# Kernel tuning notes

Hardware: AMD Instinct MI355X
Metric: run time of the kernel (lower is better)

The kernel has to match this reference:

```python
import jax, jax.numpy as jnp
import numpy as np

B, T, H, WD = 512, 168, 512, 4  # batch, seq_len, hidden_dim, WEATHER_DIM


def setup_inputs() -> dict:
    key = jax.random.key(0)
    ks = jax.random.split(key, 11)
    sc = 1.0 / np.sqrt(H)

    def u(k, shape):
        return jax.random.uniform(k, shape, jnp.float32, -sc, sc)

    return {
        "inputs": jax.random.normal(ks[0], (B, T, WD + 1), dtype=jnp.float32),
        # layer 1: input_sz=1 (counts)
        "W1": u(ks[1], (1, 4 * H)),
        "U1": u(ks[2], (H, 4 * H)),
        "V1": u(ks[3], (WD, 4 * H)),
        "b1": u(ks[4], (4 * H,)),
        # layer 2: input_sz=H
        "W2": u(ks[5], (H, 4 * H)),
        "U2": u(ks[6], (H, 4 * H)),
        "V2": u(ks[7], (WD, 4 * H)),
        "b2": u(ks[8], (4 * H,)),
        # final linear head (xavier-ish init)
        "fc_w": u(ks[9], (1, H)),
        "fc_b": jnp.zeros((1,), jnp.float32),
    }


def pew_lstm(x, w, W, U, V, b):
    """Weather-conditioned LSTM layer.
    x: [B,T,I] main input, w: [B,T,WD] weather.
    Gates = x@W + h@U + weather@V + b (weather injected each step).
    Returns hidden sequence [B,T,H]."""
    bs = x.shape[0]
    hdim = U.shape[0]
    # precompute all non-recurrent contributions once: [B,T,4H]
    pre = jnp.einsum('bti,ig->btg', x, W) + jnp.einsum('btw,wg->btg', w, V) + b

    def step(carry, pre_t):
        h, c = carry
        gates = pre_t + h @ U              # [B,4H]
        i, f, g, o = jnp.split(gates, 4, axis=-1)
        c = jax.nn.sigmoid(f) * c + jax.nn.sigmoid(i) * jnp.tanh(g)
        h = jax.nn.sigmoid(o) * jnp.tanh(c)
        return (h, c), h

    h0 = jnp.zeros((bs, hdim), x.dtype)
    (_, _), hs = jax.lax.scan(step, (h0, h0), pre.transpose(1, 0, 2))
    return hs.transpose(1, 0, 2)  # [B,T,H]


def reference(inputs, W1, U1, V1, b1, W2, U2, V2, b2, fc_w, fc_b):
    weather = inputs[:, :, :-1]   # [B,T,WD]
    counts = inputs[:, :, -1:]    # [B,T,1]
    h1 = pew_lstm(counts, weather, W1, U1, V1, b1)
    h2 = pew_lstm(h1, weather, W2, U2, V2, b2)
    out = h2.reshape(-1, h2.shape[-1]) @ fc_w.T + fc_b  # [B*T,1]
    return out.reshape(-1)
```

## Files before the change

kernel.cpp:

```cpp
#include <hip/hip_runtime.h>
#include <cstdint>
#include <cstddef>

typedef unsigned int   u32;
typedef unsigned short u16;
typedef unsigned long long u64;
typedef __attribute__((ext_vector_type(8))) short bf16x8;
typedef __attribute__((ext_vector_type(4))) float f32x4;

#define B_  512
#define T_  168
#define H_  512

#define OFF_U1P   (0u)
#define OFF_UW2P  (2u*1024*1024)
#define OFF_FLAGS (6u*1024*1024)
#define OFF_H2R   (6u*1024*1024 + 512u*1024)
#define OFF_H1_R9 (8u*1024*1024)
#define OFF_H2_R9 (12u*1024*1024)
#define OFF_H1F   (8u*1024*1024)
#define SLOT_B    (524288u)
#define OFF_H2F   (OFF_H1F + 168u*SLOT_B)
#define H_SLOT    262144u
#define NRING     8
#define FS        32
#define SMEM_SZ   (131072 + 6144 + 3072)

__device__ __forceinline__ u16 f2bf(float v){
  u32 u = __float_as_uint(v);
  return (u16)((u + 0x7fffu + ((u >> 16) & 1u)) >> 16);
}
__device__ __forceinline__ float sigm_f(float x){ return __fdividef(1.f, 1.f + __expf(-x)); }
__device__ __forceinline__ float tanh_ff(float x){
  float e = __expf(-2.f*fabsf(x));
  float t = __fdividef(1.f - e, 1.f + e);
  return (x < 0.f) ? -t : t;
}
__device__ __forceinline__ void async_cp16(const void* g, void* l){
  __builtin_amdgcn_global_load_lds((const __attribute__((address_space(1))) u32*)g,
                                   (__attribute__((address_space(3))) u32*)l, 16, 0, 0);
}
__device__ __forceinline__ void drain_vm(){
  asm volatile("s_waitcnt vmcnt(0)" ::: "memory");
}
__device__ __forceinline__ void wpoll(const int* p, bool act, int target, int& vlast){
  if (__all((!act) || (vlast >= target))) return;
  while (true){
    int v = 0x7fffffff;
    if (act) v = __hip_atomic_load(p, __ATOMIC_RELAXED, __HIP_MEMORY_SCOPE_AGENT);
    if (__all(v >= target)){ vlast = v; break; }
    __builtin_amdgcn_s_sleep(1);
  }
}
template<bool PLAIN>
__device__ __forceinline__ bf16x8 ldh(const u16* p){
  if (PLAIN) return *(const bf16x8*)p;
  union { u64 q[2]; bf16x8 v; } u;
  u.q[0] = __hip_atomic_load((const u64*)p,     __ATOMIC_RELAXED, __HIP_MEMORY_SCOPE_AGENT);
  u.q[1] = __hip_atomic_load(((const u64*)p)+1, __ATOMIC_RELAXED, __HIP_MEMORY_SCOPE_AGENT);
  return u.v;
}
__device__ __forceinline__ void ring_st16(u16* p, uint4 v){
  u64 lo = ((u64)v.y << 32) | v.x;
  u64 hi = ((u64)v.w << 32) | v.z;
  __hip_atomic_store((u64*)p,     lo, __ATOMIC_RELAXED, __HIP_MEMORY_SCOPE_AGENT);
  __hip_atomic_store(((u64*)p)+1, hi, __ATOMIC_RELAXED, __HIP_MEMORY_SCOPE_AGENT);
}

__global__ void pack_w_kernel(const float* __restrict__ U1, const float* __restrict__ W2,
                              const float* __restrict__ U2, u16* __restrict__ U1p,
                              u16* __restrict__ UW2p)
{
  int idx = blockIdx.x*256 + threadIdx.x;
  int ln = idx & 63;
  int q8 = ((ln >> 4) << 3);
  int cl = ln & 15;
  if (idx < 16*128*64) {
    int kc = idx >> 13, ng = (idx >> 6) & 127;
    int row0 = kc*32 + q8, col = ng*16 + cl;
    u16* d = U1p + (size_t)idx*8;
    #pragma unroll
    for (int j=0;j<8;j++) d[j] = f2bf(U1[(size_t)(row0+j)*2048 + col]);
  } else {
    int i2 = idx - 16*128*64;
    if (i2 >= 32*128*64) return;
    int kc = i2 >> 13, ng = (i2 >> 6) & 127;
    int row0 = kc*32 + q8, col = ng*16 + cl;
    u16* d = UW2p + (size_t)i2*8;
    #pragma unroll
    for (int j=0;j<8;j++){
      int r = row0 + j;
      float v = (r < 512) ? W2[(size_t)r*2048 + col] : U2[(size_t)(r-512)*2048 + col];
      d[j] = f2bf(v);
    }
  }
}

__global__ void init_kernel(float* __restrict__ out, const float* __restrict__ fcb,
                            int* __restrict__ flags)
{
  int i = blockIdx.x*256 + threadIdx.x;
  if (i < 1024*FS) flags[i] = 0;
  if (i < B_*T_) out[i] = fcb[0];
}

template<bool PLAIN>
__device__ __forceinline__ void l2_half(f32x4* accA, f32x4* accB, const u16* Bh,
                                        const u16* A, int bgA, int bgB, int ln)
{
  const u16* pA = A + (size_t)bgA*16*512 + (size_t)ln*8;
  const u16* pB = A + (size_t)bgB*16*512 + (size_t)ln*8;
  bf16x8 awA[8], awB[8];
  #pragma unroll
  for (int i=0;i<8;i++){
    awA[i] = ldh<PLAIN>(pA + (size_t)i*512);
    awB[i] = ldh<PLAIN>(pB + (size_t)i*512);
  }
  #pragma unroll
  for (int kc=0; kc<16; kc++){
    bf16x8 avA = awA[kc&7], avB = awB[kc&7];
    if (kc < 8){
      awA[kc&7] = ldh<PLAIN>(pA + (size_t)(kc+8)*512);
      awB[kc&7] = ldh<PLAIN>(pB + (size_t)(kc+8)*512);
    }
    const u16* bb = Bh + (size_t)kc*4*512 + (size_t)ln*8;
    #pragma unroll
    for (int ngl=0; ngl<4; ngl++){
      bf16x8 bf = *(const bf16x8*)(bb + (size_t)ngl*512);
      accA[ngl] = __builtin_amdgcn_mfma_f32_16x16x32_bf16(avA, bf, accA[ngl], 0,0,0);
      accB[ngl] = __builtin_amdgcn_mfma_f32_16x16x32_bf16(avB, bf, accB[ngl], 0,0,0);
    }
  }
}


__device__ void run_l1_fs(char* smem, int blk, const float* __restrict__ inp,
                          const float* __restrict__ W1, const float* __restrict__ V,
                          const float* __restrict__ bias, char* __restrict__ ws)
{
  u16*  Bl   = (u16*)smem;
  u16*  hlds = (u16*)(smem + 131072);
  float* wlds = (float*)(smem + 131072 + 6144);
  constexpr int RS = 40;
  const int tid = threadIdx.x, w = tid>>6, ln = tid&63, col = ln&15, quad = ln>>4;
  const int bi = blk & 7, hj = blk >> 3, h0 = hj*32, bg = bi*4 + w;

  const u16* Upak = (const u16*)(ws + OFF_U1P);
  const u16* H1f  = (const u16*)(ws + OFF_H1F);
  u16* Hw = (u16*)(ws + OFF_H1F);
  int* flag1 = (int*)(ws + OFF_FLAGS);
  const int* f1p = flag1 + (size_t)((bi*16 + (ln&15))*4 + w)*FS;
  int* myf = flag1 + (size_t)((bi*16 + hj)*4 + w)*FS;
  const bool a16 = ln < 16;
  int vl1 = 0;

  #pragma unroll
  for (int p=0;p<32;p++){
    int pid = w*32 + p, kc = pid>>3, ngl = pid&7;
    int ng = (ngl>>1)*32 + hj*2 + (ngl&1);
    async_cp16(Upak + ((size_t)(kc*128+ng)*64 + ln)*8, Bl + (size_t)pid*512);
  }
  for (int idx=tid; idx<4*32*6; idx+=256){
    int gate = idx/192, rem = idx%192, hcol = rem/6, k = rem%6;
    int gcol = gate*512 + h0 + hcol;
    wlds[idx] = (k==0)? bias[gcol] : (k<=4 ? V[(size_t)(k-1)*2048 + gcol] : W1[gcol]);
  }

  float c[8];
  #pragma unroll
  for (int i=0;i<8;i++) c[i] = 0.f;
  const f32x4 vzero = {0.f,0.f,0.f,0.f};

  __syncthreads();

  for (int t=0; t<T_; t++){
    f32x4 acc[8];
    #pragma unroll
    for (int i=0;i<8;i++) acc[i] = vzero;

    if (t > 0){
      wpoll(f1p, a16, t, vl1);
      __builtin_amdgcn_fence(__ATOMIC_ACQUIRE, "workgroup");
      const u16* ab = H1f + (size_t)(t-1)*H_SLOT + (size_t)bg*16*512 + (size_t)ln*8;
      bf16x8 aw[8];
      #pragma unroll
      for (int i=0;i<8;i++) aw[i] = ldh<true>(ab + (size_t)i*512);
      #pragma unroll
      for (int kc=0; kc<16; kc++){
        bf16x8 av = aw[kc&7];
        if (kc < 8) aw[kc&7] = ldh<true>(ab + (size_t)(kc+8)*512);
        const u16* bb = Bl + (size_t)kc*8*512 + (size_t)ln*8;
        #pragma unroll
        for (int ngl=0; ngl<8; ngl++)
          acc[ngl] = __builtin_amdgcn_mfma_f32_16x16x32_bf16(
              av, *(const bf16x8*)(bb + (size_t)ngl*512), acc[ngl], 0,0,0);
      }
    }

    float iv[4][5];
    #pragma unroll
    for (int r=0;r<4;r++){
      const float* ip = inp + ((size_t)(bi*64 + w*16 + quad*4 + r)*T_ + t)*5;
      #pragma unroll
      for (int k=0;k<5;k++) iv[r][k] = ip[k];
    }
    #pragma unroll
    for (int hg=0; hg<2; hg++){
      float wv[4][6];
      #pragma unroll
      for (int gate=0; gate<4; gate++){
        const float* wp = wlds + (size_t)(gate*32 + hg*16 + col)*6;
        #pragma unroll
        for (int k=0;k<6;k++) wv[gate][k] = wp[k];
      }
      #pragma unroll
      for (int r=0;r<4;r++){
        float gv[4];
        #pragma unroll
        for (int gate=0; gate<4; gate++){
          gv[gate] = acc[gate*2+hg][r] + wv[gate][0]
                   + iv[r][0]*wv[gate][1] + iv[r][1]*wv[gate][2]
                   + iv[r][2]*wv[gate][3] + iv[r][3]*wv[gate][4]
                   + iv[r][4]*wv[gate][5];
        }
        float ig=sigm_f(gv[0]), fg=sigm_f(gv[1]), gg=tanh_ff(gv[2]), og=sigm_f(gv[3]);
        float cn = fg*c[hg*4+r] + ig*gg;
        c[hg*4+r] = cn;
        hlds[(size_t)(w*16 + quad*4 + r)*RS + hg*16 + col] = f2bf(og*tanh_ff(cn));
      }
    }
    {
      uint4 v = *(const uint4*)&hlds[(size_t)(w*16 + (ln&15))*RS + (ln>>4)*8];
      ring_st16(Hw + (size_t)t*H_SLOT + ((size_t)(bg*16 + hj)*64 + ln)*8, v);
    }
    drain_vm();
    if (ln == 0)
      __hip_atomic_store(myf, t+1, __ATOMIC_RELAXED, __HIP_MEMORY_SCOPE_AGENT);
  }
}

template<bool H2F>
__device__ void run_l2_fs(char* smem, int blk2, const float* __restrict__ inp,
                          const float* __restrict__ V, const float* __restrict__ bias,
                          const float* __restrict__ fcw, char* __restrict__ ws,
                          float* __restrict__ out)
{
  u16*  Bl   = (u16*)smem;
  u16*  hlds = (u16*)(smem + 131072);
  float* wlds = (float*)(smem + 131072 + 6144);
  constexpr int RS = 24;
  const int tid = threadIdx.x, w = tid>>6, ln = tid&63, col = ln&15, quad = ln>>4;
  const int bi2 = blk2 & 3, hj = blk2 >> 2, h0 = hj*16;
  const int bgA = bi2*8 + w, bgB = bgA + 4;

  const u16* Upak = (const u16*)(ws + OFF_UW2P);
  const u16* H1f  = (const u16*)(ws + OFF_H1F);
  const u16* H2b  = (const u16*)(ws + (H2F ? OFF_H2F : OFF_H2R));
  u16* Hw = (u16*)(ws + (H2F ? OFF_H2F : OFF_H2R));
  int* flag1 = (int*)(ws + OFF_FLAGS);
  int* flag2 = flag1 + 512*FS;
  const int* h1f = flag1 + (size_t)((bi2*32 + (ln&31))*4 + w)*FS;
  const int* h2f = flag2 + (size_t)((bi2*32 + (ln&31))*4 + w)*FS;
  int* myf = flag2 + (size_t)((bi2*32 + hj)*4 + w)*FS;
  const bool a32 = ln < 32;
  int vlh1 = 0, vlh2 = 0;

  #pragma unroll
  for (int p=0;p<32;p++){
    int pid = w*32 + p, kc = pid>>2, ngl = pid&3;
    int ng = ngl*32 + hj;
    async_cp16(Upak + ((size_t)(kc*128+ng)*64 + ln)*8, Bl + (size_t)pid*512);
  }
  for (int idx=tid; idx<4*16*6; idx+=256){
    int gate = idx/96, rem = idx%96, hcol = rem/6, k = rem%6;
    int gcol = gate*512 + h0 + hcol;
    wlds[idx] = (k==0)? bias[gcol] : (k<=4 ? V[(size_t)(k-1)*2048 + gcol] : 0.f);
  }
  const float fcwr = fcw[h0 + col];

  float c[8];
  #pragma unroll
  for (int i=0;i<8;i++) c[i] = 0.f;
  const f32x4 vzero = {0.f,0.f,0.f,0.f};

  __syncthreads();

  for (int t=0; t<T_; t++){
    f32x4 accA[4], accB[4];
    #pragma unroll
    for (int i=0;i<4;i++){ accA[i] = vzero; accB[i] = vzero; }

    wpoll(h1f, a32, t+1, vlh1);
    __builtin_amdgcn_fence(__ATOMIC_ACQUIRE, "workgroup");
    const u16* A1 = H1f + (size_t)t*H_SLOT;
    l2_half<true>(accA, accB, Bl, A1, bgA, bgB, ln);

    if (t > 0){
      wpoll(h2f, a32, t, vlh2);
      __builtin_amdgcn_fence(__ATOMIC_ACQUIRE, "workgroup");
      const u16* A2 = H2b + (H2F ? (size_t)(t-1)*H_SLOT : (size_t)((t-1)&1)*H_SLOT);
      l2_half<H2F>(accA, accB, Bl + (size_t)16*4*512, A2, bgA, bgB, ln);
    }

    float wv[4][5];
    #pragma unroll
    for (int gate=0; gate<4; gate++){
      const float* wp = wlds + (size_t)(gate*16 + col)*6;
      #pragma unroll
      for (int k=0;k<5;k++) wv[gate][k] = wp[k];
    }
    float fcp[2][4];
    #pragma unroll
    for (int sel=0; sel<2; sel++){
      const f32x4* ac = sel ? accB : accA;
      #pragma unroll
      for (int r=0;r<4;r++){
        const float* ip = inp + ((size_t)(bi2*128 + sel*64 + w*16 + quad*4 + r)*T_ + t)*5;
        float i0=ip[0], i1=ip[1], i2=ip[2], i3=ip[3];
        float gv[4];
        #pragma unroll
        for (int gate=0; gate<4; gate++){
          gv[gate] = ac[gate][r] + wv[gate][0]
                   + i0*wv[gate][1] + i1*wv[gate][2] + i2*wv[gate][3] + i3*wv[gate][4];
        }
        float ig=sigm_f(gv[0]), fg=sigm_f(gv[1]), gg=tanh_ff(gv[2]), og=sigm_f(gv[3]);
        float cn = fg*c[sel*4+r] + ig*gg;
        c[sel*4+r] = cn;
        float h = og*tanh_ff(cn);
        fcp[sel][r] = h*fcwr;
        hlds[(size_t)(sel*64 + w*16 + quad*4 + r)*RS + col] = f2bf(h);
      }
    }
    {
      int sel = ln>>5, ch = (ln>>4)&1, m = ln&15;
      uint4 v = *(const uint4*)&hlds[(size_t)(sel*64 + w*16 + m)*RS + ch*8];
      int lp = ((hj&1)*2 + ch)*16 + m;
      int bgx = bi2*8 + sel*4 + w;
      u16* dst = Hw + (H2F ? (size_t)t*H_SLOT : (size_t)(t&1)*H_SLOT)
               + ((size_t)(bgx*16 + (hj>>1))*64 + lp)*8;
      ring_st16(dst, v);
    }
    drain_vm();
    if (ln == 0)
      __hip_atomic_store(myf, t+1, __ATOMIC_RELAXED, __HIP_MEMORY_SCOPE_AGENT);

    #pragma unroll
    for (int sel=0; sel<2; sel++){
      #pragma unroll
      for (int r=0;r<4;r++){
        float v = fcp[sel][r];
        #pragma unroll
        for (int m=1;m<16;m<<=1) v += __shfl_xor(v, m, 16);
        if (col == 0)
          atomicAdd(&out[(size_t)(bi2*128 + sel*64 + w*16 + quad*4 + r)*T_ + t], v);
      }
    }
  }
}

template<bool H2F>
__global__ void __launch_bounds__(256, 1)
lstm_main_v10(const float* __restrict__ inp, const float* __restrict__ W1,
              const float* __restrict__ V1, const float* __restrict__ b1,
              const float* __restrict__ V2, const float* __restrict__ b2,
              const float* __restrict__ fcw, char* __restrict__ ws, float* __restrict__ out)
{
  extern __shared__ char smem[];
  int blk = blockIdx.x;
  if (blk < 128) run_l1_fs(smem, blk, inp, W1, V1, b1, ws);
  else           run_l2_fs<H2F>(smem, blk-128, inp, V2, b2, fcw, ws, out);
}

__device__ void run_l1_r9(char* smem, int blk, const float* __restrict__ inp,
                          const float* __restrict__ W1, const float* __restrict__ V,
                          const float* __restrict__ bias, char* __restrict__ ws)
{
  u16*  Bl   = (u16*)smem;
  u16*  hlds = (u16*)(smem + 131072);
  float* wlds = (float*)(smem + 131072 + 6144);
  constexpr int RS = 40;
  const int tid = threadIdx.x, w = tid>>6, ln = tid&63, col = ln&15, quad = ln>>4;
  const int bi = blk & 7, hj = blk >> 3, h0 = hj*32, bg = bi*4 + w;

  const u16* Upak = (const u16*)(ws + OFF_U1P);
  const u16* H1r  = (const u16*)(ws + OFF_H1_R9);
  u16* Hw = (u16*)(ws + OFF_H1_R9);
  int* flag1 = (int*)(ws + OFF_FLAGS);
  int* flag2 = flag1 + 128*FS;
  const int* f1p = flag1 + (size_t)(bi*16 + (ln&15))*FS;
  const int* f2p = flag2 + (size_t)((bi>>1)*32 + (ln&31))*FS;
  int* myf = flag1 + (size_t)(bi*16 + hj)*FS;
  const bool a16 = ln < 16, a32 = ln < 32;
  int vl1 = 0, vlbp = 0;

  #pragma unroll
  for (int p=0;p<32;p++){
    int pid = w*32 + p, kc = pid>>3, ngl = pid&7;
    int ng = (ngl>>1)*32 + hj*2 + (ngl&1);
    async_cp16(Upak + ((size_t)(kc*128+ng)*64 + ln)*8, Bl + (size_t)pid*512);
  }
  for (int idx=tid; idx<4*32*6; idx+=256){
    int gate = idx/192, rem = idx%192, hcol = rem/6, k = rem%6;
    int gcol = gate*512 + h0 + hcol;
    wlds[idx] = (k==0)? bias[gcol] : (k<=4 ? V[(size_t)(k-1)*2048 + gcol] : W1[gcol]);
  }

  float c[8];
  #pragma unroll
  for (int i=0;i<8;i++) c[i] = 0.f;
  const f32x4 vzero = {0.f,0.f,0.f,0.f};

  for (int t=0; t<T_; t++){
    if (w == 0){
      if (t > 0)      wpoll(f1p, a16, t, vl1);
      if (t >= NRING) wpoll(f2p, a32, t-NRING+1, vlbp);
      __builtin_amdgcn_fence(__ATOMIC_ACQUIRE, "agent");
    }
    __syncthreads();

    f32x4 acc[8];
    #pragma unroll
    for (int i=0;i<8;i++) acc[i] = vzero;

    if (t > 0){
      const u16* ab = H1r + (size_t)((t-1)&7)*H_SLOT + (size_t)bg*16*512 + (size_t)ln*8;
      bf16x8 aw[8];
      #pragma unroll
      for (int i=0;i<8;i++) aw[i] = ldh<true>(ab + (size_t)i*512);
      #pragma unroll
      for (int kc=0; kc<16; kc++){
        bf16x8 av = aw[kc&7];
        if (kc < 8) aw[kc&7] = ldh<true>(ab + (size_t)(kc+8)*512);
        const u16* bb = Bl + (size_t)kc*8*512 + (size_t)ln*8;
        #pragma unroll
        for (int ngl=0; ngl<8; ngl++)
          acc[ngl] = __builtin_amdgcn_mfma_f32_16x16x32_bf16(
              av, *(const bf16x8*)(bb + (size_t)ngl*512), acc[ngl], 0,0,0);
      }
    }

    float iv[4][5];
    #pragma unroll
    for (int r=0;r<4;r++){
      const float* ip = inp + ((size_t)(bi*64 + w*16 + quad*4 + r)*T_ + t)*5;
      #pragma unroll
      for (int k=0;k<5;k++) iv[r][k] = ip[k];
    }
    #pragma unroll
    for (int hg=0; hg<2; hg++){
      float wv[4][6];
      #pragma unroll
      for (int gate=0; gate<4; gate++){
        const float* wp = wlds + (size_t)(gate*32 + hg*16 + col)*6;
        #pragma unroll
        for (int k=0;k<6;k++) wv[gate][k] = wp[k];
      }
      #pragma unroll
      for (int r=0;r<4;r++){
        float gv[4];
        #pragma unroll
        for (int gate=0; gate<4; gate++){
          gv[gate] = acc[gate*2+hg][r] + wv[gate][0]
                   + iv[r][0]*wv[gate][1] + iv[r][1]*wv[gate][2]
                   + iv[r][2]*wv[gate][3] + iv[r][3]*wv[gate][4]
                   + iv[r][4]*wv[gate][5];
        }
        float ig=sigm_f(gv[0]), fg=sigm_f(gv[1]), gg=tanh_ff(gv[2]), og=sigm_f(gv[3]);
        float cn = fg*c[hg*4+r] + ig*gg;
        c[hg*4+r] = cn;
        hlds[(size_t)(w*16 + quad*4 + r)*RS + hg*16 + col] = f2bf(og*tanh_ff(cn));
      }
    }
    {
      uint4 v = *(const uint4*)&hlds[(size_t)(w*16 + (ln&15))*RS + (ln>>4)*8];
      ring_st16(Hw + (size_t)(t&7)*H_SLOT + ((size_t)(bg*16 + hj)*64 + ln)*8, v);
    }
    __syncthreads();
    if (tid==0){
      __builtin_amdgcn_fence(__ATOMIC_RELEASE, "workgroup");
      __hip_atomic_store(myf, t+1, __ATOMIC_RELAXED, __HIP_MEMORY_SCOPE_AGENT);
    }
  }
}

__device__ void run_l2_r9(char* smem, int blk2, const float* __restrict__ inp,
                          const float* __restrict__ V, const float* __restrict__ bias,
                          const float* __restrict__ fcw, char* __restrict__ ws,
                          float* __restrict__ out)
{
  u16*  Bl   = (u16*)smem;
  u16*  hlds = (u16*)(smem + 131072);
  float* wlds = (float*)(smem + 131072 + 6144);
  constexpr int RS = 24;
  const int tid = threadIdx.x, w = tid>>6, ln = tid&63, col = ln&15, quad = ln>>4;
  const int bi2 = blk2 & 3, hj = blk2 >> 2, h0 = hj*16;
  const int bgA = bi2*8 + w, bgB = bgA + 4;

  const u16* Upak = (const u16*)(ws + OFF_UW2P);
  const u16* H1r  = (const u16*)(ws + OFF_H1_R9);
  const u16* H2r  = (const u16*)(ws + OFF_H2_R9);
  u16* Hw = (u16*)(ws + OFF_H2_R9);
  int* flag1 = (int*)(ws + OFF_FLAGS);
  int* flag2 = flag1 + 128*FS;
  const int* h1f = flag1 + (size_t)(bi2*32 + (ln&31))*FS;
  const int* h2f = flag2 + (size_t)(bi2*32 + (ln&31))*FS;
  int* myf = flag2 + (size_t)(bi2*32 + hj)*FS;
  const bool a32 = ln < 32;
  int vlh1 = 0, vlh2 = 0;

  #pragma unroll
  for (int p=0;p<32;p++){
    int pid = w*32 + p, kc = pid>>2, ngl = pid&3;
    int ng = ngl*32 + hj;
    async_cp16(Upak + ((size_t)(kc*128+ng)*64 + ln)*8, Bl + (size_t)pid*512);
  }
  for (int idx=tid; idx<4*16*6; idx+=256){
    int gate = idx/96, rem = idx%96, hcol = rem/6, k = rem%6;
    int gcol = gate*512 + h0 + hcol;
    wlds[idx] = (k==0)? bias[gcol] : (k<=4 ? V[(size_t)(k-1)*2048 + gcol] : 0.f);
  }
  const float fcwr = fcw[h0 + col];

  float c[8];
  #pragma unroll
  for (int i=0;i<8;i++) c[i] = 0.f;
  const f32x4 vzero = {0.f,0.f,0.f,0.f};

  for (int t=0; t<T_; t++){
    if (w == 0){
      wpoll(h1f, a32, t+1, vlh1);
      __builtin_amdgcn_fence(__ATOMIC_ACQUIRE, "agent");
    }
    __syncthreads();

    f32x4 accA[4], accB[4];
    #pragma unroll
    for (int i=0;i<4;i++){ accA[i] = vzero; accB[i] = vzero; }

    const u16* A1 = H1r + (size_t)(t&7)*H_SLOT;
    l2_half<true>(accA, accB, Bl, A1, bgA, bgB, ln);

    if (t > 0){
      wpoll(h2f, a32, t, vlh2);
      __builtin_amdgcn_fence(__ATOMIC_ACQUIRE, "workgroup");
      const u16* A2 = H2r + (size_t)((t-1)&1)*H_SLOT;
      l2_half<false>(accA, accB, Bl + (size_t)16*4*512, A2, bgA, bgB, ln);
    }

    float wv[4][5];
    #pragma unroll
    for (int gate=0; gate<4; gate++){
      const float* wp = wlds + (size_t)(gate*16 + col)*6;
      #pragma unroll
      for (int k=0;k<5;k++) wv[gate][k] = wp[k];
    }
    float fcp[2][4];
    #pragma unroll
    for (int sel=0; sel<2; sel++){
      const f32x4* ac = sel ? accB : accA;
      #pragma unroll
      for (int r=0;r<4;r++){
        const float* ip = inp + ((size_t)(bi2*128 + sel*64 + w*16 + quad*4 + r)*T_ + t)*5;
        float i0=ip[0], i1=ip[1], i2=ip[2], i3=ip[3];
        float gv[4];
        #pragma unroll
        for (int gate=0; gate<4; gate++){
          gv[gate] = ac[gate][r] + wv[gate][0]
                   + i0*wv[gate][1] + i1*wv[gate][2] + i2*wv[gate][3] + i3*wv[gate][4];
        }
        float ig=sigm_f(gv[0]), fg=sigm_f(gv[1]), gg=tanh_ff(gv[2]), og=sigm_f(gv[3]);
        float cn = fg*c[sel*4+r] + ig*gg;
        c[sel*4+r] = cn;
        float h = og*tanh_ff(cn);
        fcp[sel][r] = h*fcwr;
        hlds[(size_t)(sel*64 + w*16 + quad*4 + r)*RS + col] = f2bf(h);
      }
    }
    {
      int sel = ln>>5, ch = (ln>>4)&1, m = ln&15;
      uint4 v = *(const uint4*)&hlds[(size_t)(sel*64 + w*16 + m)*RS + ch*8];
      int lp = ((hj&1)*2 + ch)*16 + m;
      int bgx = bi2*8 + sel*4 + w;
      ring_st16(Hw + (size_t)(t&1)*H_SLOT + ((size_t)(bgx*16 + (hj>>1))*64 + lp)*8, v);
    }
    __syncthreads();
    if (tid==0){
      __builtin_amdgcn_fence(__ATOMIC_RELEASE, "workgroup");
      __hip_atomic_store(myf, t+1, __ATOMIC_RELAXED, __HIP_MEMORY_SCOPE_AGENT);
    }

    #pragma unroll
    for (int sel=0; sel<2; sel++){
      #pragma unroll
      for (int r=0;r<4;r++){
        float v = fcp[sel][r];
        #pragma unroll
        for (int m=1;m<16;m<<=1) v += __shfl_xor(v, m, 16);
        if (col == 0)
          atomicAdd(&out[(size_t)(bi2*128 + sel*64 + w*16 + quad*4 + r)*T_ + t], v);
      }
    }
  }
}

__global__ void __launch_bounds__(256, 1)
lstm_main_v9(const float* __restrict__ inp, const float* __restrict__ W1,
             const float* __restrict__ V1, const float* __restrict__ b1,
             const float* __restrict__ V2, const float* __restrict__ b2,
             const float* __restrict__ fcw, char* __restrict__ ws, float* __restrict__ out)
{
  extern __shared__ char smem[];
  int blk = blockIdx.x;
  if (blk < 128) run_l1_r9(smem, blk, inp, W1, V1, b1, ws);
  else           run_l2_r9(smem, blk-128, inp, V2, b2, fcw, ws, out);
}

extern "C" void kernel_launch(void* const* d_in, const int* in_sizes, int n_in,
                              void* d_out, int out_size, void* d_ws, size_t ws_size,
                              hipStream_t stream) {
  (void)in_sizes; (void)n_in; (void)out_size;
  const float* inp = (const float*)d_in[0];
  const float* W1  = (const float*)d_in[1];
  const float* U1  = (const float*)d_in[2];
  const float* V1  = (const float*)d_in[3];
  const float* b1  = (const float*)d_in[4];
  const float* W2  = (const float*)d_in[5];
  const float* U2  = (const float*)d_in[6];
  const float* V2  = (const float*)d_in[7];
  const float* b2  = (const float*)d_in[8];
  const float* fcw = (const float*)d_in[9];
  const float* fcb = (const float*)d_in[10];
  char* ws = (char*)d_ws;
  float* out = (float*)d_out;

  pack_w_kernel<<<1536, 256, 0, stream>>>(U1, W2, U2,
      (u16*)(ws + OFF_U1P), (u16*)(ws + OFF_UW2P));
  init_kernel<<<(B_*T_ + 255)/256, 256, 0, stream>>>(out, fcb, (int*)(ws + OFF_FLAGS));

  const size_t need_h1f  = (size_t)OFF_H1F + (size_t)T_*SLOT_B;
  const size_t need_both = (size_t)OFF_H2F + (size_t)T_*SLOT_B;

  if (ws_size >= need_both) {
    (void)hipFuncSetAttribute((const void*)lstm_main_v10<true>,
                              hipFuncAttributeMaxDynamicSharedMemorySize, SMEM_SZ);
    lstm_main_v10<true><<<256, 256, SMEM_SZ, stream>>>(inp, W1, V1, b1, V2, b2, fcw, ws, out);
  } else if (ws_size >= need_h1f) {
    (void)hipFuncSetAttribute((const void*)lstm_main_v10<false>,
                              hipFuncAttributeMaxDynamicSharedMemorySize, SMEM_SZ);
    lstm_main_v10<false><<<256, 256, SMEM_SZ, stream>>>(inp, W1, V1, b1, V2, b2, fcw, ws, out);
  } else {
    (void)hipFuncSetAttribute((const void*)lstm_main_v9,
                              hipFuncAttributeMaxDynamicSharedMemorySize, SMEM_SZ);
    lstm_main_v9<<<256, 256, SMEM_SZ, stream>>>(inp, W1, V1, b1, V2, b2, fcw, ws, out);
  }
}
```

Measured before the change: 2.389 ms.

## Poll per-chunk producer flags inside the K loop and add layer-1 backpressure

Replaces the single wave-wide poll before each recurrent matmul with per-K-chunk spins on the specific producer flag for each 32-column slice of h, so MFMA work can start as soon as the first slices land instead of waiting for all producers. Layer 2 does the same for both its h1 and h2 inputs. Layer 1 also gains a backpressure wait on layer-2 flags so it runs at most a fixed number of steps ahead, which keeps the h1 data it writes closer in cache. The cost is more atomic loads and fences per step, and per-chunk acquire ordering now carries correctness.

```diff
diff --git a/kernel.cpp b/kernel.cpp
--- a/kernel.cpp
+++ b/kernel.cpp
@@ -24,6 +24,7 @@
 #define H_SLOT    262144u
 #define NRING     8
 #define FS        32
+#define BPSLACK   16
 #define SMEM_SZ   (131072 + 6144 + 3072)
 
 __device__ __forceinline__ u16 f2bf(float v){
@@ -42,6 +43,31 @@
 }
 __device__ __forceinline__ void drain_vm(){
   asm volatile("s_waitcnt vmcnt(0)" ::: "memory");
+}
+
+
+__device__ __forceinline__ void spin1(const int* p, int target, int& vlast){
+  if (vlast >= target) return;
+  int v;
+  while (true){
+    v = __hip_atomic_load(p, __ATOMIC_RELAXED, __HIP_MEMORY_SCOPE_AGENT);
+    if (v >= target) break;
+    __builtin_amdgcn_s_sleep(1);
+  }
+  vlast = v;
+  __builtin_amdgcn_fence(__ATOMIC_ACQUIRE, "workgroup");
+}
+__device__ __forceinline__ void spin2(const int* p1, const int* p2, int target, int& vlast){
+  if (vlast >= target) return;
+  int v1, v2;
+  while (true){
+    v1 = __hip_atomic_load(p1, __ATOMIC_RELAXED, __HIP_MEMORY_SCOPE_AGENT);
+    v2 = __hip_atomic_load(p2, __ATOMIC_RELAXED, __HIP_MEMORY_SCOPE_AGENT);
+    if (v1 >= target && v2 >= target) break;
+    __builtin_amdgcn_s_sleep(1);
+  }
+  vlast = (v1 < v2) ? v1 : v2;
+  __builtin_amdgcn_fence(__ATOMIC_ACQUIRE, "workgroup");
 }
 __device__ __forceinline__ void wpoll(const int* p, bool act, int target, int& vlast){
   if (__all((!act) || (vlast >= target))) return;
@@ -104,39 +130,9 @@
   if (i < B_*T_) out[i] = fcb[0];
 }
 
-template<bool PLAIN>
-__device__ __forceinline__ void l2_half(f32x4* accA, f32x4* accB, const u16* Bh,
-                                        const u16* A, int bgA, int bgB, int ln)
-{
-  const u16* pA = A + (size_t)bgA*16*512 + (size_t)ln*8;
-  const u16* pB = A + (size_t)bgB*16*512 + (size_t)ln*8;
-  bf16x8 awA[8], awB[8];
-  #pragma unroll
-  for (int i=0;i<8;i++){
-    awA[i] = ldh<PLAIN>(pA + (size_t)i*512);
-    awB[i] = ldh<PLAIN>(pB + (size_t)i*512);
-  }
-  #pragma unroll
-  for (int kc=0; kc<16; kc++){
-    bf16x8 avA = awA[kc&7], avB = awB[kc&7];
-    if (kc < 8){
-      awA[kc&7] = ldh<PLAIN>(pA + (size_t)(kc+8)*512);
-      awB[kc&7] = ldh<PLAIN>(pB + (size_t)(kc+8)*512);
-    }
-    const u16* bb = Bh + (size_t)kc*4*512 + (size_t)ln*8;
-    #pragma unroll
-    for (int ngl=0; ngl<4; ngl++){
-      bf16x8 bf = *(const bf16x8*)(bb + (size_t)ngl*512);
-      accA[ngl] = __builtin_amdgcn_mfma_f32_16x16x32_bf16(avA, bf, accA[ngl], 0,0,0);
-      accB[ngl] = __builtin_amdgcn_mfma_f32_16x16x32_bf16(avB, bf, accB[ngl], 0,0,0);
-    }
-  }
-}
-
-
-__device__ void run_l1_fs(char* smem, int blk, const float* __restrict__ inp,
-                          const float* __restrict__ W1, const float* __restrict__ V,
-                          const float* __restrict__ bias, char* __restrict__ ws)
+__device__ void run_l1_v13(char* smem, int blk, const float* __restrict__ inp,
+                           const float* __restrict__ W1, const float* __restrict__ V,
+                           const float* __restrict__ bias, char* __restrict__ ws)
 {
   u16*  Bl   = (u16*)smem;
   u16*  hlds = (u16*)(smem + 131072);
@@ -149,10 +145,14 @@
   const u16* H1f  = (const u16*)(ws + OFF_H1F);
   u16* Hw = (u16*)(ws + OFF_H1F);
   int* flag1 = (int*)(ws + OFF_FLAGS);
-  const int* f1p = flag1 + (size_t)((bi*16 + (ln&15))*4 + w)*FS;
+  int* flag2 = flag1 + 512*FS;
   int* myf = flag1 + (size_t)((bi*16 + hj)*4 + w)*FS;
-  const bool a16 = ln < 16;
-  int vl1 = 0;
+  const int* f2p = flag2 + (size_t)(((bi>>1)*32 + (ln&31))*4 + w)*FS;
+  const bool a32 = ln < 32;
+  int vl1[16];
+  #pragma unroll
+  for (int i=0;i<16;i++) vl1[i] = 0;
+  int vlbp = 0;
 
   #pragma unroll
   for (int p=0;p<32;p++){
@@ -179,16 +179,20 @@
     for (int i=0;i<8;i++) acc[i] = vzero;
 
     if (t > 0){
-      wpoll(f1p, a16, t, vl1);
-      __builtin_amdgcn_fence(__ATOMIC_ACQUIRE, "workgroup");
       const u16* ab = H1f + (size_t)(t-1)*H_SLOT + (size_t)bg*16*512 + (size_t)ln*8;
       bf16x8 aw[8];
       #pragma unroll
-      for (int i=0;i<8;i++) aw[i] = ldh<true>(ab + (size_t)i*512);
+      for (int i=0;i<8;i++){
+        spin1(flag1 + ((size_t)(bi*16 + i)*4 + w)*FS, t, vl1[i]);
+        aw[i] = ldh<true>(ab + (size_t)i*512);
+      }
       #pragma unroll
       for (int kc=0; kc<16; kc++){
         bf16x8 av = aw[kc&7];
-        if (kc < 8) aw[kc&7] = ldh<true>(ab + (size_t)(kc+8)*512);
+        if (kc < 8){
+          spin1(flag1 + ((size_t)(bi*16 + kc+8)*4 + w)*FS, t, vl1[kc+8]);
+          aw[kc&7] = ldh<true>(ab + (size_t)(kc+8)*512);
+        }
         const u16* bb = Bl + (size_t)kc*8*512 + (size_t)ln*8;
         #pragma unroll
         for (int ngl=0; ngl<8; ngl++)
@@ -229,6 +233,7 @@
         hlds[(size_t)(w*16 + quad*4 + r)*RS + hg*16 + col] = f2bf(og*tanh_ff(cn));
       }
     }
+    if (t >= BPSLACK) wpoll(f2p, a32, t-BPSLACK+1, vlbp);
     {
       uint4 v = *(const uint4*)&hlds[(size_t)(w*16 + (ln&15))*RS + (ln>>4)*8];
       ring_st16(Hw + (size_t)t*H_SLOT + ((size_t)(bg*16 + hj)*64 + ln)*8, v);
@@ -240,10 +245,10 @@
 }
 
 template<bool H2F>
-__device__ void run_l2_fs(char* smem, int blk2, const float* __restrict__ inp,
-                          const float* __restrict__ V, const float* __restrict__ bias,
-                          const float* __restrict__ fcw, char* __restrict__ ws,
-                          float* __restrict__ out)
+__device__ void run_l2_v13(char* smem, int blk2, const float* __restrict__ inp,
+                           const float* __restrict__ V, const float* __restrict__ bias,
+                           const float* __restrict__ fcw, char* __restrict__ ws,
+                           float* __restrict__ out)
 {
   u16*  Bl   = (u16*)smem;
   u16*  hlds = (u16*)(smem + 131072);
@@ -259,11 +264,10 @@
   u16* Hw = (u16*)(ws + (H2F ? OFF_H2F : OFF_H2R));
   int* flag1 = (int*)(ws + OFF_FLAGS);
   int* flag2 = flag1 + 512*FS;
-  const int* h1f = flag1 + (size_t)((bi2*32 + (ln&31))*4 + w)*FS;
-  const int* h2f = flag2 + (size_t)((bi2*32 + (ln&31))*4 + w)*FS;
   int* myf = flag2 + (size_t)((bi2*32 + hj)*4 + w)*FS;
-  const bool a32 = ln < 32;
-  int vlh1 = 0, vlh2 = 0;
+  int vlA1[16], vlA2[16];
+  #pragma unroll
+  for (int i=0;i<16;i++){ vlA1[i] = 0; vlA2[i] = 0; }
 
   #pragma unroll
   for (int p=0;p<32;p++){
@@ -290,16 +294,65 @@
     #pragma unroll
     for (int i=0;i<4;i++){ accA[i] = vzero; accB[i] = vzero; }
 
-    wpoll(h1f, a32, t+1, vlh1);
-    __builtin_amdgcn_fence(__ATOMIC_ACQUIRE, "workgroup");
-    const u16* A1 = H1f + (size_t)t*H_SLOT;
-    l2_half<true>(accA, accB, Bl, A1, bgA, bgB, ln);
-
+    {
+      const u16* A1 = H1f + (size_t)t*H_SLOT;
+      const u16* pA = A1 + (size_t)bgA*16*512 + (size_t)ln*8;
+      const u16* pB = A1 + (size_t)bgB*16*512 + (size_t)ln*8;
+      bf16x8 awA[8], awB[8];
+      #pragma unroll
+      for (int i=0;i<8;i++){
+        spin2(flag1 + ((size_t)((2*bi2  )*16 + i)*4 + w)*FS,
+              flag1 + ((size_t)((2*bi2+1)*16 + i)*4 + w)*FS, t+1, vlA1[i]);
+        awA[i] = ldh<true>(pA + (size_t)i*512);
+        awB[i] = ldh<true>(pB + (size_t)i*512);
+      }
+      #pragma unroll
+      for (int kc=0; kc<16; kc++){
+        bf16x8 avA = awA[kc&7], avB = awB[kc&7];
+        if (kc < 8){
+          spin2(flag1 + ((size_t)((2*bi2  )*16 + kc+8)*4 + w)*FS,
+                flag1 + ((size_t)((2*bi2+1)*16 + kc+8)*4 + w)*FS, t+1, vlA1[kc+8]);
+          awA[kc&7] = ldh<true>(pA + (size_t)(kc+8)*512);
+          awB[kc&7] = ldh<true>(pB + (size_t)(kc+8)*512);
+        }
+        const u16* bb = Bl + (size_t)kc*4*512 + (size_t)ln*8;
+        #pragma unroll
+        for (int ngl=0; ngl<4; ngl++){
+          bf16x8 bf = *(const bf16x8*)(bb + (size_t)ngl*512);
+          accA[ngl] = __builtin_amdgcn_mfma_f32_16x16x32_bf16(avA, bf, accA[ngl], 0,0,0);
+          accB[ngl] = __builtin_amdgcn_mfma_f32_16x16x32_bf16(avB, bf, accB[ngl], 0,0,0);
+        }
+      }
+    }
     if (t > 0){
-      wpoll(h2f, a32, t, vlh2);
-      __builtin_amdgcn_fence(__ATOMIC_ACQUIRE, "workgroup");
       const u16* A2 = H2b + (H2F ? (size_t)(t-1)*H_SLOT : (size_t)((t-1)&1)*H_SLOT);
-      l2_half<H2F>(accA, accB, Bl + (size_t)16*4*512, A2, bgA, bgB, ln);
+      const u16* pA = A2 + (size_t)bgA*16*512 + (size_t)ln*8;
+      const u16* pB = A2 + (size_t)bgB*16*512 + (size_t)ln*8;
+      bf16x8 awA[8], awB[8];
+      #pragma unroll
+      for (int i=0;i<8;i++){
+        spin2(flag2 + ((size_t)(bi2*32 + 2*i  )*4 + w)*FS,
+              flag2 + ((size_t)(bi2*32 + 2*i+1)*4 + w)*FS, t, vlA2[i]);
+        awA[i] = ldh<H2F>(pA + (size_t)i*512);
+        awB[i] = ldh<H2F>(pB + (size_t)i*512);
+      }
+      #pragma unroll
+      for (int kc=0; kc<16; kc++){
+        bf16x8 avA = awA[kc&7], avB = awB[kc&7];
+        if (kc < 8){
+          spin2(flag2 + ((size_t)(bi2*32 + 2*(kc+8)  )*4 + w)*FS,
+                flag2 + ((size_t)(bi2*32 + 2*(kc+8)+1)*4 + w)*FS, t, vlA2[kc+8]);
+          awA[kc&7] = ldh<H2F>(pA + (size_t)(kc+8)*512);
+          awB[kc&7] = ldh<H2F>(pB + (size_t)(kc+8)*512);
+        }
+        const u16* bb = Bl + (size_t)(16+kc)*4*512 + (size_t)ln*8;
+        #pragma unroll
+        for (int ngl=0; ngl<4; ngl++){
+          bf16x8 bf = *(const bf16x8*)(bb + (size_t)ngl*512);
+          accA[ngl] = __builtin_amdgcn_mfma_f32_16x16x32_bf16(avA, bf, accA[ngl], 0,0,0);
+          accB[ngl] = __builtin_amdgcn_mfma_f32_16x16x32_bf16(avB, bf, accB[ngl], 0,0,0);
+        }
+      }
     }
 
     float wv[4][5];
@@ -360,15 +413,15 @@
 
 template<bool H2F>
 __global__ void __launch_bounds__(256, 1)
-lstm_main_v10(const float* __restrict__ inp, const float* __restrict__ W1,
+lstm_main_v13(const float* __restrict__ inp, const float* __restrict__ W1,
               const float* __restrict__ V1, const float* __restrict__ b1,
               const float* __restrict__ V2, const float* __restrict__ b2,
               const float* __restrict__ fcw, char* __restrict__ ws, float* __restrict__ out)
 {
   extern __shared__ char smem[];
   int blk = blockIdx.x;
-  if (blk < 128) run_l1_fs(smem, blk, inp, W1, V1, b1, ws);
-  else           run_l2_fs<H2F>(smem, blk-128, inp, V2, b2, fcw, ws, out);
+  if (blk < 128) run_l1_v13(smem, blk, inp, W1, V1, b1, ws);
+  else           run_l2_v13<H2F>(smem, blk-128, inp, V2, b2, fcw, ws, out);
 }
 
 __device__ void run_l1_r9(char* smem, int blk, const float* __restrict__ inp,
@@ -479,6 +532,35 @@
     if (tid==0){
       __builtin_amdgcn_fence(__ATOMIC_RELEASE, "workgroup");
       __hip_atomic_store(myf, t+1, __ATOMIC_RELAXED, __HIP_MEMORY_SCOPE_AGENT);
+    }
+  }
+}
+
+template<bool PLAIN>
+__device__ __forceinline__ void l2_half(f32x4* accA, f32x4* accB, const u16* Bh,
+                                        const u16* A, int bgA, int bgB, int ln)
+{
+  const u16* pA = A + (size_t)bgA*16*512 + (size_t)ln*8;
+  const u16* pB = A + (size_t)bgB*16*512 + (size_t)ln*8;
+  bf16x8 awA[8], awB[8];
+  #pragma unroll
+  for (int i=0;i<8;i++){
+    awA[i] = ldh<PLAIN>(pA + (size_t)i*512);
+    awB[i] = ldh<PLAIN>(pB + (size_t)i*512);
+  }
+  #pragma unroll
+  for (int kc=0; kc<16; kc++){
+    bf16x8 avA = awA[kc&7], avB = awB[kc&7];
+    if (kc < 8){
+      awA[kc&7] = ldh<PLAIN>(pA + (size_t)(kc+8)*512);
+      awB[kc&7] = ldh<PLAIN>(pB + (size_t)(kc+8)*512);
+    }
+    const u16* bb = Bh + (size_t)kc*4*512 + (size_t)ln*8;
+    #pragma unroll
+    for (int ngl=0; ngl<4; ngl++){
+      bf16x8 bf = *(const bf16x8*)(bb + (size_t)ngl*512);
+      accA[ngl] = __builtin_amdgcn_mfma_f32_16x16x32_bf16(avA, bf, accA[ngl], 0,0,0);
+      accB[ngl] = __builtin_amdgcn_mfma_f32_16x16x32_bf16(avB, bf, accB[ngl], 0,0,0);
     }
   }
 }
@@ -604,10 +686,10 @@
 }
 
 __global__ void __launch_bounds__(256, 1)
-lstm_main_v9(const float* __restrict__ inp, const float* __restrict__ W1,
-             const float* __restrict__ V1, const float* __restrict__ b1,
-             const float* __restrict__ V2, const float* __restrict__ b2,
-             const float* __restrict__ fcw, char* __restrict__ ws, float* __restrict__ out)
+lstm_main_v9fb(const float* __restrict__ inp, const float* __restrict__ W1,
+               const float* __restrict__ V1, const float* __restrict__ b1,
+               const float* __restrict__ V2, const float* __restrict__ b2,
+               const float* __restrict__ fcw, char* __restrict__ ws, float* __restrict__ out)
 {
   extern __shared__ char smem[];
   int blk = blockIdx.x;
@@ -641,16 +723,16 @@
   const size_t need_both = (size_t)OFF_H2F + (size_t)T_*SLOT_B;
 
   if (ws_size >= need_both) {
-    (void)hipFuncSetAttribute((const void*)lstm_main_v10<true>,
+    (void)hipFuncSetAttribute((const void*)lstm_main_v13<true>,
                               hipFuncAttributeMaxDynamicSharedMemorySize, SMEM_SZ);
-    lstm_main_v10<true><<<256, 256, SMEM_SZ, stream>>>(inp, W1, V1, b1, V2, b2, fcw, ws, out);
+    lstm_main_v13<true><<<256, 256, SMEM_SZ, stream>>>(inp, W1, V1, b1, V2, b2, fcw, ws, out);
   } else if (ws_size >= need_h1f) {
-    (void)hipFuncSetAttribute((const void*)lstm_main_v10<false>,
+    (void)hipFuncSetAttribute((const void*)lstm_main_v13<false>,
                               hipFuncAttributeMaxDynamicSharedMemorySize, SMEM_SZ);
-    lstm_main_v10<false><<<256, 256, SMEM_SZ, stream>>>(inp, W1, V1, b1, V2, b2, fcw, ws, out);
+    lstm_main_v13<false><<<256, 256, SMEM_SZ, stream>>>(inp, W1, V1, b1, V2, b2, fcw, ws, out);
   } else {
-    (void)hipFuncSetAttribute((const void*)lstm_main_v9,
+    (void)hipFuncSetAttribute((const void*)lstm_main_v9fb,
                               hipFuncAttributeMaxDynamicSharedMemorySize, SMEM_SZ);
-    lstm_main_v9<<<256, 256, SMEM_SZ, stream>>>(inp, W1, V1, b1, V2, b2, fcw, ws, out);
-  }
-}
+    lstm_main_v9fb<<<256, 256, SMEM_SZ, stream>>>(inp, W1, V1, b1, V2, b2, fcw, ws, out);
+  }
+}
```

Result: slower. 2.445 ms (+2.4%).
